# Optimization experiments

Measured on AMD Instinct MI355X. Metric: run time of the kernel, lower is better.

Reference implementation:

```python
import jax, jax.numpy as jnp
import numpy as np

L, H, DIN, T, B = 3, 512, 512, 256, 64


def _lstm_layer(x, m, h0, c0, Wih, Whh, b, reverse):
    # x: [T,B,Din], m: [T,B,1], h0/c0: [B,H], Wih: [4H,Din], Whh: [4H,H], b: [4H]
    def step(carry, xm):
        h, c = carry
        xt, mt = xm
        gates = xt @ Wih.T + h @ Whh.T + b  # [B,4H]
        i, f, g, o = jnp.split(gates, 4, axis=-1)
        c_n = (jax.nn.sigmoid(f) * c + jax.nn.sigmoid(i) * jnp.tanh(g)) * mt
        h_n = jax.nn.sigmoid(o) * jnp.tanh(c_n) * mt
        return (h_n, c_n), h_n
    (hT, cT), hs = jax.lax.scan(step, (h0, c0), (x, m), reverse=reverse)
    return hs, hT, cT


def setup_inputs():
    key = jax.random.key(0)
    ks = jax.random.split(key, 16)
    s = 0.05
    return {
        "x": jax.random.normal(ks[0], (T, B, DIN), jnp.float32),
        "masks": (jax.random.uniform(ks[1], (T, B, 1)) < 0.9).astype(jnp.float32),
        "f_Wih0": jax.random.normal(ks[2], (4 * H, DIN), jnp.float32) * s,
        "f_Wih_rest": jax.random.normal(ks[3], (L - 1, 4 * H, 2 * H), jnp.float32) * s,
        "f_Whh": jax.random.normal(ks[4], (L, 4 * H, H), jnp.float32) * s,
        "f_b": jnp.zeros((L, 4 * H), jnp.float32),
        "b_Wih0": jax.random.normal(ks[5], (4 * H, DIN), jnp.float32) * s,
        "b_Wih_rest": jax.random.normal(ks[6], (L - 1, 4 * H, 2 * H), jnp.float32) * s,
        "b_Whh": jax.random.normal(ks[7], (L, 4 * H, H), jnp.float32) * s,
        "b_b": jnp.zeros((L, 4 * H), jnp.float32),
        "f_init": jax.random.normal(ks[8], (L, 2, H), jnp.float32) * s,
        "b_init": jax.random.normal(ks[9], (L, 2, H), jnp.float32) * s,
        "proj_W": jax.random.normal(ks[10], (L - 1, 2 * H, 2 * H), jnp.float32) * s,
        "proj_b": jnp.zeros((L - 1, 2 * H), jnp.float32),
    }


def reference(x, masks, f_Wih0, f_Wih_rest, f_Whh, f_b, b_Wih0, b_Wih_rest, b_Whh, b_b,
              f_init, b_init, proj_W, proj_b):
    batch = x.shape[1]
    inp = x
    h_n, c_n = [], []
    for layer in range(L):
        Wih_f = f_Wih0 if layer == 0 else f_Wih_rest[layer - 1]
        Wih_b = b_Wih0 if layer == 0 else b_Wih_rest[layer - 1]
        h0f = jnp.broadcast_to(f_init[layer, 0], (batch, H))
        c0f = jnp.broadcast_to(f_init[layer, 1], (batch, H))
        h0b = jnp.broadcast_to(b_init[layer, 0], (batch, H))
        c0b = jnp.broadcast_to(b_init[layer, 1], (batch, H))
        fout, fh, fc = _lstm_layer(inp, masks, h0f, c0f, Wih_f, f_Whh[layer], f_b[layer], False)
        bout, bh, bc = _lstm_layer(inp, masks, h0b, c0b, Wih_b, b_Whh[layer], b_b[layer], True)
        h_n += [fh, bh]
        c_n += [fc, bc]
        out = jnp.concatenate([fout, bout], axis=-1)  # [T,B,2H]
        if layer > 0:
            g = jax.nn.sigmoid(out @ proj_W[layer - 1].T + proj_b[layer - 1])
            out = g * out + (1.0 - g) * inp
        inp = out
    return out, jnp.stack(h_n, 0), jnp.stack(c_n, 0)
```

## Files before the change

### kernel.cpp

```cpp
#include <hip/hip_runtime.h>

typedef __attribute__((ext_vector_type(8))) short short8;
typedef __attribute__((ext_vector_type(4))) float f32x4;

#define MFMA_B16(a, b, c) __builtin_amdgcn_mfma_f32_16x16x32_bf16((a), (b), (c), 0, 0, 0)

#define TSTEPS 256
#define NBATCH 64
#define HID    512
#define NBLK   32
#define UB     16
#define HSLOT  (NBATCH * HID)

__device__ __forceinline__ unsigned short f2bf(float f) {
  unsigned int u = __float_as_uint(f);
  u += 0x7fffu + ((u >> 16) & 1u);
  return (unsigned short)(u >> 16);
}
__device__ __forceinline__ float bf2f(unsigned short s) {
  return __uint_as_float(((unsigned int)s) << 16);
}
__device__ __forceinline__ float sigm(float x) { return 1.0f / (1.0f + __expf(-x)); }
__device__ __forceinline__ float tanhf_(float x) {
  float xc = fminf(fmaxf(x, -15.0f), 15.0f);
  float e = __expf(2.0f * xc);
  return (e - 1.0f) / (e + 1.0f);
}

__device__ __forceinline__ unsigned int ld_flag(const unsigned int* p) {
  return __hip_atomic_load(p, __ATOMIC_RELAXED, __HIP_MEMORY_SCOPE_AGENT);
}
__device__ __forceinline__ void st_flag(unsigned int* p, unsigned int v) {
  __hip_atomic_store(p, v, __ATOMIC_RELAXED, __HIP_MEMORY_SCOPE_AGENT);
}
__device__ __forceinline__ void st_u64(unsigned long long* p, unsigned long long v) {
  __hip_atomic_store(p, v, __ATOMIC_RELAXED, __HIP_MEMORY_SCOPE_AGENT);
}
__device__ __forceinline__ short8 ld_llc16(const unsigned short* p) {
  union { unsigned long long q[2]; short8 s; } u;
  unsigned long long* a = (unsigned long long*)p;
  u.q[0] = __hip_atomic_load(a,     __ATOMIC_RELAXED, __HIP_MEMORY_SCOPE_AGENT);
  u.q[1] = __hip_atomic_load(a + 1, __ATOMIC_RELAXED, __HIP_MEMORY_SCOPE_AGENT);
  return u.s;
}

__global__ void cvt_all(const float* __restrict__ x,
                        const float* __restrict__ fWih0, const float* __restrict__ bWih0,
                        const float* __restrict__ fWihR, const float* __restrict__ bWihR,
                        const float* __restrict__ fWhh,  const float* __restrict__ bWhh,
                        const float* __restrict__ projW,
                        unsigned short* __restrict__ dst)
{
  const int tot = 6815744;
  for (int i = blockIdx.x * blockDim.x + threadIdx.x; i < tot; i += gridDim.x * blockDim.x) {
    const float* src; int r;
    if      (i < 2097152) { src = x;                 r = i; }
    else if (i < 2359296) { src = fWih0;             r = i - 2097152; }
    else if (i < 2621440) { src = bWih0;             r = i - 2359296; }
    else if (i < 3145728) { src = fWihR;             r = i - 2621440; }
    else if (i < 3670016) { src = bWihR;             r = i - 3145728; }
    else if (i < 4194304) { src = fWihR + 2097152;   r = i - 3670016; }
    else if (i < 4718592) { src = bWihR + 2097152;   r = i - 4194304; }
    else if (i < 5505024) { src = fWhh;              r = i - 4718592; }
    else if (i < 6291456) { src = bWhh;              r = i - 5505024; }
    else                  { src = projW;             r = i - 6291456; }
    f32x4 v = ((const f32x4*)src)[r];
    union { unsigned short u[4]; unsigned long long q; } o;
    o.u[0] = f2bf(v[0]); o.u[1] = f2bf(v[1]); o.u[2] = f2bf(v[2]); o.u[3] = f2bf(v[3]);
    ((unsigned long long*)dst)[i] = o.q;
  }
}

template<int K>
__global__ __launch_bounds__(256)
void gates_gemm(const unsigned short* __restrict__ act,
                const unsigned short* __restrict__ wcat,
                const float* __restrict__ bias_f,
                const float* __restrict__ bias_b,
                unsigned short* __restrict__ gates)
{
  const int lane = threadIdx.x & 63;
  const int wave = threadIdx.x >> 6;
  const int n = lane & 15, kb = lane >> 4;
  const int t0 = blockIdx.x * 2;
  const int rbase = blockIdx.y * 256 + wave * 64;

  f32x4 acc[2][4][4];
  #pragma unroll
  for (int mt = 0; mt < 4; ++mt) {
    f32x4 bi;
    #pragma unroll
    for (int i = 0; i < 4; ++i) {
      int r = rbase + mt * 16 + kb * 4 + i;
      bi[i] = (r < 2048) ? bias_f[r] : bias_b[r - 2048];
    }
    #pragma unroll
    for (int nt = 0; nt < 4; ++nt) { acc[0][mt][nt] = bi; acc[1][mt][nt] = bi; }
  }
  const unsigned short* wrow  = wcat + (size_t)(rbase + n) * K + kb * 8;
  const unsigned short* arow0 = act + ((size_t)t0 * 64 + n) * K + kb * 8;
  const unsigned short* arow1 = arow0 + (size_t)64 * K;
  #pragma unroll 2
  for (int ks = 0; ks < K / 32; ++ks) {
    short8 af[4], b0[4], b1[4];
    #pragma unroll
    for (int mt = 0; mt < 4; ++mt) af[mt] = *(const short8*)(wrow + (size_t)mt * 16 * K + ks * 32);
    #pragma unroll
    for (int nt = 0; nt < 4; ++nt) {
      b0[nt] = *(const short8*)(arow0 + (size_t)nt * 16 * K + ks * 32);
      b1[nt] = *(const short8*)(arow1 + (size_t)nt * 16 * K + ks * 32);
    }
    #pragma unroll
    for (int mt = 0; mt < 4; ++mt)
      #pragma unroll
      for (int nt = 0; nt < 4; ++nt) {
        acc[0][mt][nt] = MFMA_B16(af[mt], b0[nt], acc[0][mt][nt]);
        acc[1][mt][nt] = MFMA_B16(af[mt], b1[nt], acc[1][mt][nt]);
      }
  }
  #pragma unroll
  for (int t2 = 0; t2 < 2; ++t2) {
    unsigned short* gbase = gates + (size_t)(t0 + t2) * 4096 * 64;
    #pragma unroll
    for (int mt = 0; mt < 4; ++mt)
      #pragma unroll
      for (int i = 0; i < 4; ++i) {
        int r = rbase + mt * 16 + kb * 4 + i;
        #pragma unroll
        for (int nt = 0; nt < 4; ++nt)
          gbase[(size_t)r * 64 + nt * 16 + n] = f2bf(acc[t2][mt][nt][i]);
      }
  }
}

template<int DIN, int GXP>
__global__ __launch_bounds__(256, 1)
void scan_kernel(const unsigned short* __restrict__ act_in,
                 const unsigned short* __restrict__ gates,
                 unsigned short* __restrict__ act_out,
                 const unsigned short* __restrict__ wih_f,
                 const unsigned short* __restrict__ wih_b,
                 const unsigned short* __restrict__ whh_f,
                 const unsigned short* __restrict__ whh_b,
                 const float* __restrict__ bias_f,
                 const float* __restrict__ bias_b,
                 const float* __restrict__ init_f,
                 const float* __restrict__ init_b,
                 const float* __restrict__ masks,
                 unsigned short* hb,
                 unsigned int* bar,
                 float* out_h, float* out_c)
{
  const int bid  = blockIdx.x;
  const int dir  = bid >> 5;
  const int jb   = bid & (NBLK - 1);
  const int j0   = jb * UB;
  const int lane = threadIdx.x & 63;
  const int wave = threadIdx.x >> 6;
  const int n    = lane & 15;
  const int kb   = lane >> 4;
  const int u    = n & 7;
  const bool hif = (n >= 8);

  const unsigned short* wih = dir ? wih_b : wih_f;
  const unsigned short* whh = dir ? whh_b : whh_f;
  const float* bias = dir ? bias_b : bias_f;
  const float* init = dir ? init_b : init_f;
  const unsigned int* mypoll = bar + ((dir * 32 + jb) << 5) + (lane & 31);
  unsigned int* scat = bar + ((dir * 32 + (lane & 31)) << 5) + jb;
  unsigned short* hbd = hb + dir * (2 * HSLOT);
  float* oh = out_h + dir * (NBATCH * HID);
  float* oc = out_c + dir * (NBATCH * HID);

  int wr[4];
  wr[0] = hif ? (512 + j0 + u) : (j0 + u);
  wr[1] = wr[0] + 8;
  wr[2] = wr[0] + 1024;
  wr[3] = wr[0] + 1032;

  float bb[4];
  const unsigned short* wihp[4];
  #pragma unroll
  for (int q = 0; q < 4; ++q) {
    bb[q] = bias[wr[q]];
    wihp[q] = wih + (size_t)wr[q] * DIN + kb * 8;
  }

  __shared__ short8 wlds[16 * 4 * 64];
  __shared__ unsigned short lsm[2][NBATCH * UB];

  for (int g = threadIdx.x; g < 4096; g += 256) {
    int n_ = g & 15, kb_ = (g >> 4) & 3, q_ = (g >> 6) & 3, ks_ = g >> 8;
    int grow = ((n_ >= 8) ? 512 : 0) + j0 + (n_ & 7) + (q_ & 1) * 8 + (q_ >> 1) * 1024;
    wlds[g] = *(const short8*)(whh + (size_t)grow * HID + ks_ * 32 + kb_ * 8);
  }

  float cs[2][4];
  #pragma unroll
  for (int uh = 0; uh < 2; ++uh)
    #pragma unroll
    for (int i = 0; i < 4; ++i)
      cs[uh][i] = init[512 + j0 + uh * 8 + u];

  __syncthreads();

  if (wave == 0) {
    union { unsigned short us[16]; unsigned long long q[4]; } iv;
    #pragma unroll
    for (int k = 0; k < 16; ++k) iv.us[k] = f2bf(init[j0 + k]);
    unsigned long long* hd = (unsigned long long*)(hbd + jb * (NBATCH * UB) + lane * UB);
    #pragma unroll
    for (int k = 0; k < 4; ++k) st_u64(hd + k, iv.q[k]);
    asm volatile("s_waitcnt vmcnt(0)" ::: "memory");
    if (lane < 32) st_flag(scat, 1u);
  }

  f32x4 acc_e[4], acc_o[4];

  auto wih_load = [&](int tstep) {
    #pragma unroll
    for (int q = 0; q < 4; ++q) {
      acc_e[q] = (f32x4){bb[q], bb[q], bb[q], bb[q]};
      acc_o[q] = (f32x4){0.f, 0.f, 0.f, 0.f};
    }
    const int tt2 = dir ? (TSTEPS - 1 - tstep) : tstep;
    const unsigned short* arow = act_in + ((size_t)tt2 * NBATCH + wave * 16 + n) * DIN + kb * 8;
    #pragma unroll
    for (int kt = 0; kt < DIN / 32; kt += 2) {
      short8 a0 = *(const short8*)(arow + kt * 32);
      short8 a1 = *(const short8*)(arow + kt * 32 + 32);
      #pragma unroll
      for (int q = 0; q < 4; ++q) {
        acc_e[q] = MFMA_B16(a0, *(const short8*)(wihp[q] + kt * 32), acc_e[q]);
        acc_o[q] = MFMA_B16(a1, *(const short8*)(wihp[q] + kt * 32 + 32), acc_o[q]);
      }
    }
  };

  if (!GXP) wih_load(0);

  for (int t = 0; t < TSTEPS; ++t) {
    const int tt = dir ? (TSTEPS - 1 - t) : t;

    f32x4 mk = *(const f32x4*)(masks + tt * NBATCH + wave * 16 + kb * 4);
    if (GXP) {
      const unsigned short* gb = gates + ((size_t)tt * 4096 + dir * 2048) * 64 + wave * 16 + kb * 4;
      #pragma unroll
      for (int q = 0; q < 4; ++q) {
        union { unsigned long long q8; unsigned short us[4]; } gv;
        gv.q8 = *(const unsigned long long*)(gb + (size_t)wr[q] * 64);
        acc_e[q] = (f32x4){bf2f(gv.us[0]), bf2f(gv.us[1]), bf2f(gv.us[2]), bf2f(gv.us[3])};
        acc_o[q] = (f32x4){0.f, 0.f, 0.f, 0.f};
      }
    }

    {
      const unsigned int tgt = t + 1;
      while (!__all((int)(ld_flag(mypoll) >= tgt)))
        __builtin_amdgcn_s_sleep(1);
    }

    {
      const unsigned short* hrow = hbd + (t & 1) * HSLOT
                                 + (kb >> 1) * 1024 + (kb & 1) * 8 + (wave * 16 + n) * UB;
      short8 hf[16];
      #pragma unroll
      for (int ks = 0; ks < 16; ++ks) hf[ks] = ld_llc16(hrow + ks * 2048);
      #pragma unroll
      for (int ks = 0; ks < 16; ++ks) {
        f32x4* ac = (ks & 1) ? acc_o : acc_e;
        #pragma unroll
        for (int q = 0; q < 4; ++q)
          ac[q] = MFMA_B16(hf[ks], wlds[(ks * 4 + q) * 64 + lane], ac[q]);
      }
    }

    #pragma unroll
    for (int uh = 0; uh < 2; ++uh) {
      f32x4 aif = acc_e[uh] + acc_o[uh];
      f32x4 ago = acc_e[2 + uh] + acc_o[2 + uh];
      f32x4 oif, ogo;
      #pragma unroll
      for (int r = 0; r < 4; ++r) {
        oif[r] = __shfl_xor(aif[r], 8, 64);
        ogo[r] = __shfl_xor(ago[r], 8, 64);
      }
      #pragma unroll
      for (int i = 0; i < 4; ++i) {
        float vi = hif ? oif[i] : aif[i];
        float vf = hif ? aif[i] : oif[i];
        float vg = hif ? ogo[i] : ago[i];
        float vo = hif ? ago[i] : ogo[i];
        float cn = (sigm(vf) * cs[uh][i] + sigm(vi) * tanhf_(vg)) * mk[i];
        float hvv = sigm(vo) * tanhf_(cn) * mk[i];
        cs[uh][i] = cn;
        if (!hif) {
          const int b = wave * 16 + kb * 4 + i;
          lsm[t & 1][b * UB + uh * 8 + u] = f2bf(hvv);
          if (t == TSTEPS - 1) {
            oh[b * HID + j0 + uh * 8 + u] = hvv;
            oc[b * HID + j0 + uh * 8 + u] = cn;
          }
        }
      }
    }

    __syncthreads();

    if (wave == 0) {
      if (t + 1 < TSTEPS) {
        const unsigned long long* lq = (const unsigned long long*)lsm[t & 1];
        unsigned long long q0 = lq[lane * 4 + 0];
        unsigned long long q1 = lq[lane * 4 + 1];
        unsigned long long q2 = lq[lane * 4 + 2];
        unsigned long long q3 = lq[lane * 4 + 3];
        unsigned long long* hd = (unsigned long long*)
            (hbd + ((t + 1) & 1) * HSLOT + jb * (NBATCH * UB) + lane * UB);
        st_u64(hd + 0, q0); st_u64(hd + 1, q1);
        st_u64(hd + 2, q2); st_u64(hd + 3, q3);
        asm volatile("s_waitcnt vmcnt(0)" ::: "memory");
        if (lane < 32) st_flag(scat, (unsigned int)(t + 2));
      }
    } else if (wave == 1) {
      const unsigned long long* lq = (const unsigned long long*)lsm[t & 1];
      union { unsigned long long q[2]; short8 s; } p0, p1;
      p0.q[0] = lq[lane * 4 + 0]; p0.q[1] = lq[lane * 4 + 1];
      p1.q[0] = lq[lane * 4 + 2]; p1.q[1] = lq[lane * 4 + 3];
      short8* ar = (short8*)(act_out + ((size_t)tt * NBATCH + lane) * (2 * HID) + dir * HID + j0);
      ar[0] = p0.s;
      ar[1] = p1.s;
    }

    if (!GXP && t + 1 < TSTEPS) wih_load(t + 1);
  }
}

template<int FINAL>
__global__ __launch_bounds__(256)
void highway_kernel(const unsigned short* __restrict__ raw,
                    unsigned short* __restrict__ inp,
                    const unsigned short* __restrict__ pw,
                    const float* __restrict__ pb,
                    float* __restrict__ outf)
{
  const int lane = threadIdx.x & 63;
  const int wave = threadIdx.x >> 6;
  const int n = lane & 15, kb = lane >> 4;
  const int r0 = blockIdx.x * 64 + wave * 16;
  const int c0 = blockIdx.y * 64;
  f32x4 acc[4];
  #pragma unroll
  for (int nt = 0; nt < 4; ++nt) {
    float b = pb[c0 + nt * 16 + n];
    acc[nt] = (f32x4){b, b, b, b};
  }
  const unsigned short* arow = raw + (r0 + n) * 1024 + kb * 8;
  #pragma unroll 4
  for (int kt = 0; kt < 32; ++kt) {
    short8 a = *(const short8*)(arow + kt * 32);
    #pragma unroll
    for (int nt = 0; nt < 4; ++nt) {
      short8 b = *(const short8*)(pw + (c0 + nt * 16 + n) * 1024 + kt * 32 + kb * 8);
      acc[nt] = MFMA_B16(a, b, acc[nt]);
    }
  }
  #pragma unroll
  for (int nt = 0; nt < 4; ++nt)
    #pragma unroll
    for (int i = 0; i < 4; ++i) {
      int row = r0 + kb * 4 + i;
      int col = c0 + nt * 16 + n;
      float g = sigm(acc[nt][i]);
      float rv = bf2f(raw[row * 1024 + col]);
      float iv = bf2f(inp[row * 1024 + col]);
      float ov = g * rv + (1.0f - g) * iv;
      if (FINAL) outf[row * 1024 + col] = ov;
      else       inp[row * 1024 + col] = f2bf(ov);
    }
}

extern "C" void kernel_launch(void* const* d_in, const int* in_sizes, int n_in,
                              void* d_out, int out_size, void* d_ws, size_t ws_size,
                              hipStream_t stream) {
  const float* x     = (const float*)d_in[0];
  const float* masks = (const float*)d_in[1];
  const float* fWih0 = (const float*)d_in[2];
  const float* fWihR = (const float*)d_in[3];
  const float* fWhh  = (const float*)d_in[4];
  const float* fb    = (const float*)d_in[5];
  const float* bWih0 = (const float*)d_in[6];
  const float* bWihR = (const float*)d_in[7];
  const float* bWhh  = (const float*)d_in[8];
  const float* bbias = (const float*)d_in[9];
  const float* fInit = (const float*)d_in[10];
  const float* bInit = (const float*)d_in[11];
  const float* projW = (const float*)d_in[12];
  const float* projB = (const float*)d_in[13];
  float* out = (float*)d_out;

  char* ws = (char*)d_ws;
  unsigned short* bufA  = (unsigned short*)(ws + 0);
  unsigned short* bufB  = (unsigned short*)(ws + 33554432);
  unsigned short* xbf   = (unsigned short*)(ws + 67108864);
  unsigned short* wcat0 = (unsigned short*)(ws + 83886080);
  unsigned short* wcat1 = (unsigned short*)(ws + 88080384);
  unsigned short* wcat2 = (unsigned short*)(ws + 96468992);
  unsigned short* whf   = (unsigned short*)(ws + 104857600);
  unsigned short* whb   = (unsigned short*)(ws + 111149056);
  unsigned short* pj    = (unsigned short*)(ws + 117440512);
  unsigned short* hbuf  = (unsigned short*)(ws + 121634816);
  unsigned int*   bar   = (unsigned int*)(ws + 121896960);
  unsigned short* gates = (unsigned short*)(ws + 121921536);
  const bool gx = ws_size >= 256139264ull;

  hipMemsetAsync(bar, 0, 24576, stream);
  cvt_all<<<1024, 256, 0, stream>>>(x, fWih0, bWih0, fWihR, bWihR, fWhh, bWhh, projW, xbf);

  float* outH = out + 16777216;
  float* outC = out + 16777216 + 6*64*512;

  if (gx) {
    gates_gemm<512><<<dim3(128, 16), 256, 0, stream>>>(xbf, wcat0, fb, bbias, gates);
    scan_kernel<512, 1><<<64, 256, 0, stream>>>(
        xbf, gates, bufA,
        wcat0, wcat0 + 2048*512, whf, whb,
        fb, bbias, fInit, bInit, masks, hbuf, bar,
        outH, outC);
    gates_gemm<1024><<<dim3(128, 16), 256, 0, stream>>>(bufA, wcat1, fb + 2048, bbias + 2048, gates);
    scan_kernel<1024, 1><<<64, 256, 0, stream>>>(
        bufA, gates, bufB,
        wcat1, wcat1 + 2048*1024, whf + 2048*512, whb + 2048*512,
        fb + 2048, bbias + 2048, fInit + 1024, bInit + 1024, masks, hbuf, bar + 2048,
        outH + 2*64*512, outC + 2*64*512);
    highway_kernel<0><<<dim3(256, 16), 256, 0, stream>>>(bufB, bufA, pj, projB, nullptr);
    gates_gemm<1024><<<dim3(128, 16), 256, 0, stream>>>(bufA, wcat2, fb + 4096, bbias + 4096, gates);
    scan_kernel<1024, 1><<<64, 256, 0, stream>>>(
        bufA, gates, bufB,
        wcat2, wcat2 + 2048*1024, whf + 2*2048*512, whb + 2*2048*512,
        fb + 4096, bbias + 4096, fInit + 2048, bInit + 2048, masks, hbuf, bar + 4096,
        outH + 4*64*512, outC + 4*64*512);
    highway_kernel<1><<<dim3(256, 16), 256, 0, stream>>>(bufB, bufA, pj + 1024*1024, projB + 1024, out);
  } else {
    scan_kernel<512, 0><<<64, 256, 0, stream>>>(
        xbf, nullptr, bufA,
        wcat0, wcat0 + 2048*512, whf, whb,
        fb, bbias, fInit, bInit, masks, hbuf, bar,
        outH, outC);
    scan_kernel<1024, 0><<<64, 256, 0, stream>>>(
        bufA, nullptr, bufB,
        wcat1, wcat1 + 2048*1024, whf + 2048*512, whb + 2048*512,
        fb + 2048, bbias + 2048, fInit + 1024, bInit + 1024, masks, hbuf, bar + 2048,
        outH + 2*64*512, outC + 2*64*512);
    highway_kernel<0><<<dim3(256, 16), 256, 0, stream>>>(bufB, bufA, pj, projB, nullptr);
    scan_kernel<1024, 0><<<64, 256, 0, stream>>>(
        bufA, nullptr, bufB,
        wcat2, wcat2 + 2048*1024, whf + 2*2048*512, whb + 2*2048*512,
        fb + 4096, bbias + 4096, fInit + 2048, bInit + 2048, masks, hbuf, bar + 4096,
        outH + 4*64*512, outC + 4*64*512);
    highway_kernel<1><<<dim3(256, 16), 256, 0, stream>>>(bufB, bufA, pj + 1024*1024, projB + 1024, out);
  }
}
```

Measured before the change: 6.051 ms.

## Add wider-tile scan kernel with fewer blocks for precomputed-gates path

```diff
diff --git a/kernel.cpp b/kernel.cpp
--- a/kernel.cpp
+++ b/kernel.cpp
@@ -133,10 +133,174 @@
   }
 }
 
-template<int DIN, int GXP>
+__global__ __launch_bounds__(256, 1)
+void scan2_kernel(const unsigned short* __restrict__ gates,
+                  unsigned short* __restrict__ act_out,
+                  const unsigned short* __restrict__ whh_f,
+                  const unsigned short* __restrict__ whh_b,
+                  const float* __restrict__ init_f,
+                  const float* __restrict__ init_b,
+                  const float* __restrict__ masks,
+                  unsigned short* hb,
+                  unsigned int* bar,
+                  float* out_h, float* out_c)
+{
+  const int bid  = blockIdx.x;
+  const int dir  = bid >> 4;
+  const int jb   = bid & 15;
+  const int j0   = jb * 32;
+  const int lane = threadIdx.x & 63;
+  const int wave = threadIdx.x >> 6;
+  const int n    = lane & 15;
+  const int kb   = lane >> 4;
+  const int u    = n & 7;
+  const bool hif = (n >= 8);
+
+  const unsigned short* whh = dir ? whh_b : whh_f;
+  const float* init = dir ? init_b : init_f;
+  const unsigned int* mypoll = bar + ((dir * 16 + jb) << 5) + (lane & 15);
+  unsigned int* scat = bar + ((dir * 16 + (lane & 15)) << 5) + jb;
+  unsigned short* hbd = hb + dir * (2 * HSLOT);
+  float* oh = out_h + dir * (NBATCH * HID);
+  float* oc = out_c + dir * (NBATCH * HID);
+
+  int wr[8];
+  #pragma unroll
+  for (int q = 0; q < 4; ++q) {
+    int unit = j0 + q * 8 + u;
+    wr[q]     = hif ? (512 + unit) : unit;
+    wr[4 + q] = wr[q] + 1024;
+  }
+
+  __shared__ short8 wlds[16 * 8 * 64];
+  __shared__ unsigned short lsm[2][NBATCH * 32];
+
+  for (int g = threadIdx.x; g < 8192; g += 256) {
+    int n_ = g & 15, kb_ = (g >> 4) & 3, q_ = (g >> 6) & 7, ks_ = g >> 9;
+    int unit = j0 + (q_ & 3) * 8 + (n_ & 7);
+    int grow = ((n_ >= 8) ? 512 : 0) + unit + (q_ >> 2) * 1024;
+    wlds[g] = *(const short8*)(whh + (size_t)grow * HID + ks_ * 32 + kb_ * 8);
+  }
+
+  float cs[4][4];
+  #pragma unroll
+  for (int uh = 0; uh < 4; ++uh)
+    #pragma unroll
+    for (int i = 0; i < 4; ++i)
+      cs[uh][i] = init[512 + j0 + uh * 8 + u];
+
+  __syncthreads();
+
+  if (wave == 0) {
+    union { unsigned short us[32]; unsigned long long q[8]; } iv;
+    #pragma unroll
+    for (int k = 0; k < 32; ++k) iv.us[k] = f2bf(init[j0 + k]);
+    unsigned long long* hd = (unsigned long long*)(hbd + jb * 2048 + lane * 32);
+    #pragma unroll
+    for (int k = 0; k < 8; ++k) st_u64(hd + k, iv.q[k]);
+    asm volatile("s_waitcnt vmcnt(0)" ::: "memory");
+    if (lane < 16) st_flag(scat, 1u);
+  }
+
+  f32x4 acc_e[8], acc_o[8];
+
+  for (int t = 0; t < TSTEPS; ++t) {
+    const int tt = dir ? (TSTEPS - 1 - t) : t;
+
+    f32x4 mk = *(const f32x4*)(masks + tt * NBATCH + wave * 16 + kb * 4);
+    {
+      const unsigned short* gb = gates + ((size_t)tt * 4096 + dir * 2048) * 64 + wave * 16 + kb * 4;
+      #pragma unroll
+      for (int q = 0; q < 8; ++q) {
+        union { unsigned long long q8; unsigned short us[4]; } gv;
+        gv.q8 = *(const unsigned long long*)(gb + (size_t)wr[q] * 64);
+        acc_e[q] = (f32x4){bf2f(gv.us[0]), bf2f(gv.us[1]), bf2f(gv.us[2]), bf2f(gv.us[3])};
+        acc_o[q] = (f32x4){0.f, 0.f, 0.f, 0.f};
+      }
+    }
+
+    {
+      const unsigned int tgt = t + 1;
+      while (!__all((int)(ld_flag(mypoll) >= tgt)))
+        __builtin_amdgcn_s_sleep(1);
+    }
+
+    {
+      const unsigned short* hrow = hbd + (t & 1) * HSLOT + (wave * 16 + n) * 32 + kb * 8;
+      short8 hf[16];
+      #pragma unroll
+      for (int ks = 0; ks < 16; ++ks)
+        asm volatile("global_load_dwordx4 %0, %1, off sc0 sc1"
+                     : "=&v"(hf[ks]) : "v"(hrow + ks * 2048));
+      asm volatile("s_waitcnt vmcnt(0)"
+                   : "+v"(hf[0]), "+v"(hf[1]), "+v"(hf[2]), "+v"(hf[3]),
+                     "+v"(hf[4]), "+v"(hf[5]), "+v"(hf[6]), "+v"(hf[7]),
+                     "+v"(hf[8]), "+v"(hf[9]), "+v"(hf[10]), "+v"(hf[11]),
+                     "+v"(hf[12]), "+v"(hf[13]), "+v"(hf[14]), "+v"(hf[15])
+                   :: "memory");
+      __builtin_amdgcn_sched_barrier(0);
+      #pragma unroll
+      for (int ks = 0; ks < 16; ++ks) {
+        f32x4* ac = (ks & 1) ? acc_o : acc_e;
+        #pragma unroll
+        for (int q = 0; q < 8; ++q)
+          ac[q] = MFMA_B16(hf[ks], wlds[(ks * 8 + q) * 64 + lane], ac[q]);
+      }
+    }
+
+    #pragma unroll
+    for (int uh = 0; uh < 4; ++uh) {
+      f32x4 aif = acc_e[uh] + acc_o[uh];
+      f32x4 ago = acc_e[4 + uh] + acc_o[4 + uh];
+      f32x4 oif, ogo;
+      #pragma unroll
+      for (int r = 0; r < 4; ++r) {
+        oif[r] = __shfl_xor(aif[r], 8, 64);
+        ogo[r] = __shfl_xor(ago[r], 8, 64);
+      }
+      #pragma unroll
+      for (int i = 0; i < 4; ++i) {
+        float vi = hif ? oif[i] : aif[i];
+        float vf = hif ? aif[i] : oif[i];
+        float vg = hif ? ogo[i] : ago[i];
+        float vo = hif ? ago[i] : ogo[i];
+        float cn = (sigm(vf) * cs[uh][i] + sigm(vi) * tanhf_(vg)) * mk[i];
+        float hvv = sigm(vo) * tanhf_(cn) * mk[i];
+        cs[uh][i] = cn;
+        if (!hif) {
+          const int b = wave * 16 + kb * 4 + i;
+          lsm[t & 1][b * 32 + uh * 8 + u] = f2bf(hvv);
+          if (t == TSTEPS - 1) {
+            oh[b * HID + j0 + uh * 8 + u] = hvv;
+            oc[b * HID + j0 + uh * 8 + u] = cn;
+          }
+        }
+      }
+    }
+
+    __syncthreads();
+
+    if (wave == 0) {
+      if (t + 1 < TSTEPS) {
+        const unsigned long long* lq = (const unsigned long long*)lsm[t & 1] + lane * 8;
+        unsigned long long* hd = (unsigned long long*)
+            (hbd + ((t + 1) & 1) * HSLOT + jb * 2048 + lane * 32);
+        #pragma unroll
+        for (int k = 0; k < 8; ++k) st_u64(hd + k, lq[k]);
+        asm volatile("s_waitcnt vmcnt(0)" ::: "memory");
+        if (lane < 16) st_flag(scat, (unsigned int)(t + 2));
+      }
+    } else if (wave == 1) {
+      const short8* ls = (const short8*)lsm[t & 1] + lane * 4;
+      short8* ar = (short8*)(act_out + ((size_t)tt * NBATCH + lane) * (2 * HID) + dir * HID + j0);
+      ar[0] = ls[0]; ar[1] = ls[1]; ar[2] = ls[2]; ar[3] = ls[3];
+    }
+  }
+}
+
+template<int DIN>
 __global__ __launch_bounds__(256, 1)
 void scan_kernel(const unsigned short* __restrict__ act_in,
-                 const unsigned short* __restrict__ gates,
                  unsigned short* __restrict__ act_out,
                  const unsigned short* __restrict__ wih_f,
                  const unsigned short* __restrict__ wih_b,
@@ -147,19 +311,16 @@
                  const float* __restrict__ init_f,
                  const float* __restrict__ init_b,
                  const float* __restrict__ masks,
-                 unsigned short* hb,
-                 unsigned int* bar,
+                 unsigned short* hb, unsigned int* bar,
                  float* out_h, float* out_c)
 {
-  const int bid  = blockIdx.x;
-  const int dir  = bid >> 5;
-  const int jb   = bid & (NBLK - 1);
-  const int j0   = jb * UB;
+  const int bid = blockIdx.x;
+  const int dir = bid >> 5;
+  const int jb = bid & (NBLK - 1);
+  const int j0 = jb * UB;
   const int lane = threadIdx.x & 63;
   const int wave = threadIdx.x >> 6;
-  const int n    = lane & 15;
-  const int kb   = lane >> 4;
-  const int u    = n & 7;
+  const int n = lane & 15, kb = lane >> 4, u = n & 7;
   const bool hif = (n >= 8);
 
   const unsigned short* wih = dir ? wih_b : wih_f;
@@ -174,10 +335,7 @@
 
   int wr[4];
   wr[0] = hif ? (512 + j0 + u) : (j0 + u);
-  wr[1] = wr[0] + 8;
-  wr[2] = wr[0] + 1024;
-  wr[3] = wr[0] + 1032;
-
+  wr[1] = wr[0] + 8; wr[2] = wr[0] + 1024; wr[3] = wr[0] + 1032;
   float bb[4];
   const unsigned short* wihp[4];
   #pragma unroll
@@ -185,25 +343,19 @@
     bb[q] = bias[wr[q]];
     wihp[q] = wih + (size_t)wr[q] * DIN + kb * 8;
   }
-
   __shared__ short8 wlds[16 * 4 * 64];
-  __shared__ unsigned short lsm[2][NBATCH * UB];
-
+  __shared__ unsigned short lsm[NBATCH * UB];
   for (int g = threadIdx.x; g < 4096; g += 256) {
     int n_ = g & 15, kb_ = (g >> 4) & 3, q_ = (g >> 6) & 3, ks_ = g >> 8;
     int grow = ((n_ >= 8) ? 512 : 0) + j0 + (n_ & 7) + (q_ & 1) * 8 + (q_ >> 1) * 1024;
     wlds[g] = *(const short8*)(whh + (size_t)grow * HID + ks_ * 32 + kb_ * 8);
   }
-
   float cs[2][4];
   #pragma unroll
   for (int uh = 0; uh < 2; ++uh)
     #pragma unroll
-    for (int i = 0; i < 4; ++i)
-      cs[uh][i] = init[512 + j0 + uh * 8 + u];
-
+    for (int i = 0; i < 4; ++i) cs[uh][i] = init[512 + j0 + uh * 8 + u];
   __syncthreads();
-
   if (wave == 0) {
     union { unsigned short us[16]; unsigned long long q[4]; } iv;
     #pragma unroll
@@ -214,9 +366,7 @@
     asm volatile("s_waitcnt vmcnt(0)" ::: "memory");
     if (lane < 32) st_flag(scat, 1u);
   }
-
   f32x4 acc_e[4], acc_o[4];
-
   auto wih_load = [&](int tstep) {
     #pragma unroll
     for (int q = 0; q < 4; ++q) {
@@ -236,30 +386,14 @@
       }
     }
   };
-
-  if (!GXP) wih_load(0);
-
+  wih_load(0);
   for (int t = 0; t < TSTEPS; ++t) {
     const int tt = dir ? (TSTEPS - 1 - t) : t;
-
     f32x4 mk = *(const f32x4*)(masks + tt * NBATCH + wave * 16 + kb * 4);
-    if (GXP) {
-      const unsigned short* gb = gates + ((size_t)tt * 4096 + dir * 2048) * 64 + wave * 16 + kb * 4;
-      #pragma unroll
-      for (int q = 0; q < 4; ++q) {
-        union { unsigned long long q8; unsigned short us[4]; } gv;
-        gv.q8 = *(const unsigned long long*)(gb + (size_t)wr[q] * 64);
-        acc_e[q] = (f32x4){bf2f(gv.us[0]), bf2f(gv.us[1]), bf2f(gv.us[2]), bf2f(gv.us[3])};
-        acc_o[q] = (f32x4){0.f, 0.f, 0.f, 0.f};
-      }
-    }
-
     {
       const unsigned int tgt = t + 1;
-      while (!__all((int)(ld_flag(mypoll) >= tgt)))
-        __builtin_amdgcn_s_sleep(1);
-    }
-
+      while (!__all((int)(ld_flag(mypoll) >= tgt))) __builtin_amdgcn_s_sleep(1);
+    }
     {
       const unsigned short* hrow = hbd + (t & 1) * HSLOT
                                  + (kb >> 1) * 1024 + (kb & 1) * 8 + (wave * 16 + n) * UB;
@@ -274,7 +408,6 @@
           ac[q] = MFMA_B16(hf[ks], wlds[(ks * 4 + q) * 64 + lane], ac[q]);
       }
     }
-
     #pragma unroll
     for (int uh = 0; uh < 2; ++uh) {
       f32x4 aif = acc_e[uh] + acc_o[uh];
@@ -296,7 +429,7 @@
         cs[uh][i] = cn;
         if (!hif) {
           const int b = wave * 16 + kb * 4 + i;
-          lsm[t & 1][b * UB + uh * 8 + u] = f2bf(hvv);
+          lsm[b * UB + uh * 8 + u] = f2bf(hvv);
           if (t == TSTEPS - 1) {
             oh[b * HID + j0 + uh * 8 + u] = hvv;
             oc[b * HID + j0 + uh * 8 + u] = cn;
@@ -304,16 +437,12 @@
         }
       }
     }
-
     __syncthreads();
-
     if (wave == 0) {
+      const unsigned long long* lq = (const unsigned long long*)lsm;
+      unsigned long long q0 = lq[lane * 4 + 0], q1 = lq[lane * 4 + 1];
+      unsigned long long q2 = lq[lane * 4 + 2], q3 = lq[lane * 4 + 3];
       if (t + 1 < TSTEPS) {
-        const unsigned long long* lq = (const unsigned long long*)lsm[t & 1];
-        unsigned long long q0 = lq[lane * 4 + 0];
-        unsigned long long q1 = lq[lane * 4 + 1];
-        unsigned long long q2 = lq[lane * 4 + 2];
-        unsigned long long q3 = lq[lane * 4 + 3];
         unsigned long long* hd = (unsigned long long*)
             (hbd + ((t + 1) & 1) * HSLOT + jb * (NBATCH * UB) + lane * UB);
         st_u64(hd + 0, q0); st_u64(hd + 1, q1);
@@ -321,17 +450,12 @@
         asm volatile("s_waitcnt vmcnt(0)" ::: "memory");
         if (lane < 32) st_flag(scat, (unsigned int)(t + 2));
       }
-    } else if (wave == 1) {
-      const unsigned long long* lq = (const unsigned long long*)lsm[t & 1];
       union { unsigned long long q[2]; short8 s; } p0, p1;
-      p0.q[0] = lq[lane * 4 + 0]; p0.q[1] = lq[lane * 4 + 1];
-      p1.q[0] = lq[lane * 4 + 2]; p1.q[1] = lq[lane * 4 + 3];
+      p0.q[0] = q0; p0.q[1] = q1; p1.q[0] = q2; p1.q[1] = q3;
       short8* ar = (short8*)(act_out + ((size_t)tt * NBATCH + lane) * (2 * HID) + dir * HID + j0);
-      ar[0] = p0.s;
-      ar[1] = p1.s;
-    }
-
-    if (!GXP && t + 1 < TSTEPS) wih_load(t + 1);
+      ar[0] = p0.s; ar[1] = p1.s;
+    }
+    if (t + 1 < TSTEPS) wih_load(t + 1);
   }
 }
 
@@ -421,42 +545,31 @@
 
   if (gx) {
     gates_gemm<512><<<dim3(128, 16), 256, 0, stream>>>(xbf, wcat0, fb, bbias, gates);
-    scan_kernel<512, 1><<<64, 256, 0, stream>>>(
-        xbf, gates, bufA,
-        wcat0, wcat0 + 2048*512, whf, whb,
-        fb, bbias, fInit, bInit, masks, hbuf, bar,
-        outH, outC);
+    scan2_kernel<<<32, 256, 0, stream>>>(
+        gates, bufA, whf, whb, fInit, bInit, masks, hbuf, bar, outH, outC);
     gates_gemm<1024><<<dim3(128, 16), 256, 0, stream>>>(bufA, wcat1, fb + 2048, bbias + 2048, gates);
-    scan_kernel<1024, 1><<<64, 256, 0, stream>>>(
-        bufA, gates, bufB,
-        wcat1, wcat1 + 2048*1024, whf + 2048*512, whb + 2048*512,
+    scan2_kernel<<<32, 256, 0, stream>>>(
+        gates, bufB, whf + 2048*512, whb + 2048*512, fInit + 1024, bInit + 1024,
+        masks, hbuf, bar + 2048, outH + 2*64*512, outC + 2*64*512);
+    highway_kernel<0><<<dim3(256, 16), 256, 0, stream>>>(bufB, bufA, pj, projB, nullptr);
+    gates_gemm<1024><<<dim3(128, 16), 256, 0, stream>>>(bufA, wcat2, fb + 4096, bbias + 4096, gates);
+    scan2_kernel<<<32, 256, 0, stream>>>(
+        gates, bufB, whf + 2*2048*512, whb + 2*2048*512, fInit + 2048, bInit + 2048,
+        masks, hbuf, bar + 4096, outH + 4*64*512, outC + 4*64*512);
+    highway_kernel<1><<<dim3(256, 16), 256, 0, stream>>>(bufB, bufA, pj + 1024*1024, projB + 1024, out);
+  } else {
+    scan_kernel<512><<<64, 256, 0, stream>>>(
+        xbf, bufA, wcat0, wcat0 + 2048*512, whf, whb,
+        fb, bbias, fInit, bInit, masks, hbuf, bar, outH, outC);
+    scan_kernel<1024><<<64, 256, 0, stream>>>(
+        bufA, bufB, wcat1, wcat1 + 2048*1024, whf + 2048*512, whb + 2048*512,
         fb + 2048, bbias + 2048, fInit + 1024, bInit + 1024, masks, hbuf, bar + 2048,
         outH + 2*64*512, outC + 2*64*512);
     highway_kernel<0><<<dim3(256, 16), 256, 0, stream>>>(bufB, bufA, pj, projB, nullptr);
-    gates_gemm<1024><<<dim3(128, 16), 256, 0, stream>>>(bufA, wcat2, fb + 4096, bbias + 4096, gates);
-    scan_kernel<1024, 1><<<64, 256, 0, stream>>>(
-        bufA, gates, bufB,
-        wcat2, wcat2 + 2048*1024, whf + 2*2048*512, whb + 2*2048*512,
+    scan_kernel<1024><<<64, 256, 0, stream>>>(
+        bufA, bufB, wcat2, wcat2 + 2048*1024, whf + 2*2048*512, whb + 2*2048*512,
         fb + 4096, bbias + 4096, fInit + 2048, bInit + 2048, masks, hbuf, bar + 4096,
         outH + 4*64*512, outC + 4*64*512);
     highway_kernel<1><<<dim3(256, 16), 256, 0, stream>>>(bufB, bufA, pj + 1024*1024, projB + 1024, out);
-  } else {
-    scan_kernel<512, 0><<<64, 256, 0, stream>>>(
-        xbf, nullptr, bufA,
-        wcat0, wcat0 + 2048*512, whf, whb,
-        fb, bbias, fInit, bInit, masks, hbuf, bar,
-        outH, outC);
-    scan_kernel<1024, 0><<<64, 256, 0, stream>>>(
-        bufA, nullptr, bufB,
-        wcat1, wcat1 + 2048*1024, whf + 2048*512, whb + 2048*512,
-        fb + 2048, bbias + 2048, fInit + 1024, bInit + 1024, masks, hbuf, bar + 2048,
-        outH + 2*64*512, outC + 2*64*512);
-    highway_kernel<0><<<dim3(256, 16), 256, 0, stream>>>(bufB, bufA, pj, projB, nullptr);
-    scan_kernel<1024, 0><<<64, 256, 0, stream>>>(
-        bufA, nullptr, bufB,
-        wcat2, wcat2 + 2048*1024, whf + 2*2048*512, whb + 2*2048*512,
-        fb + 4096, bbias + 4096, fInit + 2048, bInit + 2048, masks, hbuf, bar + 4096,
-        outH + 4*64*512, outC + 4*64*512);
-    highway_kernel<1><<<dim3(256, 16), 256, 0, stream>>>(bufB, bufA, pj + 1024*1024, projB + 1024, out);
-  }
-}
+  }
+}
```

New measurement: 10.25 ms. +69.4%, slower.
